# Optimization experiments

Measured on AMD Instinct MI355X. Metric: run time of the kernel, lower is better.

## Reference

```python
import jax, jax.numpy as jnp
import numpy as np

NUM_TIMESTEPS = 32
TOPK = 8


def setup_inputs() -> dict:
    key = jax.random.key(0)
    k = jax.random.split(key, 6)
    B, N, T, C = 16, 512, 32, 128
    r, d = C // 4, C // 2
    x_wav = jax.random.normal(k[0], (B, N, T, C), dtype=jnp.float32)
    # 1x1 Conv2d over channel dim == linear: weight [out_c, in_c]
    Ws = jax.random.normal(k[1], (r, C), dtype=jnp.float32) * 0.05   # W_shared, no bias
    Wphi = jax.random.normal(k[2], (C, r), dtype=jnp.float32) * 0.05
    b_phi = jnp.zeros((C,), dtype=jnp.float32)
    Wmu = jax.random.normal(k[3], (1, r), dtype=jnp.float32) * 0.05
    b_mu = jnp.zeros((1,), dtype=jnp.float32)
    WQ = jax.random.normal(k[4], (d, C), dtype=jnp.float32) * 0.05
    WK = jax.random.normal(k[5], (d, C), dtype=jnp.float32) * 0.05
    return {"x_wav": x_wav, "Ws": Ws, "Wphi": Wphi, "b_phi": b_phi,
            "Wmu": Wmu, "b_mu": b_mu, "WQ": WQ, "WK": WK}


def _row_topk(A, k):
    # keep the k largest entries per row (ties resolved by threshold;
    # with continuous sigmoid scores this matches torch's scatter mask)
    kth = jax.lax.top_k(A, k)[0][..., -1:]
    return A * (A >= kth).astype(A.dtype)


def reference(x_wav, Ws, Wphi, b_phi, Wmu, b_mu, WQ, WK):
    B, N, T, C = x_wav.shape
    T_delta = min(NUM_TIMESTEPS, T)
    X_w = x_wav[:, :, T - T_delta:, :]                       # [B,N,Td,C]
    # channel attention gate from time-averaged features
    avg = jnp.mean(X_w, axis=2, keepdims=True)               # [B,N,1,C]
    z_ca = jax.nn.relu(jnp.einsum('bntc,rc->bntr', avg, Ws))
    w = jax.nn.sigmoid(jnp.einsum('bntr,cr->bntc', z_ca, Wphi) + b_phi)  # [B,N,1,C]
    X_hat = X_w * w                                          # [B,N,Td,C]
    # temporal attention pooling
    z_ta = jax.nn.relu(jnp.einsum('bntc,rc->bntr', X_hat, Ws))
    logits = (jnp.einsum('bntr,or->bnto', z_ta, Wmu) + b_mu)[..., 0]     # [B,N,Td]
    alpha = jax.nn.softmax(logits, axis=2)
    X_c = jnp.einsum('bnt,bntc->bnc', alpha, X_hat)          # [B,N,C]
    # directed QK attention
    Q = jnp.einsum('bnc,dc->bnd', X_c, WQ)
    K = jnp.einsum('bnc,dc->bnd', X_c, WK)
    scale = jnp.sqrt(jnp.asarray(Q.shape[-1], dtype=X_c.dtype))
    E_f = jnp.einsum('bnd,bmd->bnm', Q, K) / scale
    E_b = jnp.einsum('bnd,bmd->bnm', K, Q) / scale
    S_f = _row_topk(jax.nn.sigmoid(E_f), TOPK)
    S_b = _row_topk(jax.nn.sigmoid(E_b), TOPK)
    return S_f, S_b
```

## Files before the change

### kernel.cpp

```cpp
#include <hip/hip_runtime.h>
#include <math.h>

#define BB 16
#define NN 512
#define TT 32
#define CC 128
#define RR 32
#define DD 64

__device__ __forceinline__ float dot_np16(const float* __restrict__ a,
                                          const float* __restrict__ b, int n) {
    float lane[16];
#pragma unroll
    for (int l = 0; l < 16; ++l) lane[l] = 0.0f;
    for (int i = 0; i < n; i += 16) {
#pragma unroll
        for (int l = 0; l < 16; ++l)
            lane[l] = __fmaf_rn(a[i + l], b[i + l], lane[l]);
    }
    float m[8], p[4];
#pragma unroll
    for (int i = 0; i < 8; ++i) m[i] = __fadd_rn(lane[i], lane[i + 8]);
#pragma unroll
    for (int i = 0; i < 4; ++i) p[i] = __fadd_rn(m[i], m[i + 4]);
    float q0 = __fadd_rn(p[0], p[2]);
    float q1 = __fadd_rn(p[1], p[3]);
    return __fadd_rn(q0, q1);
}

__device__ __forceinline__ float reduce_np16(const float (&lane)[16]) {
    float m[8], p[4];
#pragma unroll
    for (int i = 0; i < 8; ++i) m[i] = __fadd_rn(lane[i], lane[i + 8]);
#pragma unroll
    for (int i = 0; i < 4; ++i) p[i] = __fadd_rn(m[i], m[i + 4]);
    float q0 = __fadd_rn(p[0], p[2]);
    float q1 = __fadd_rn(p[1], p[3]);
    return __fadd_rn(q0, q1);
}

#define XS2 132

__global__ __launch_bounds__(256) void k1(const float* __restrict__ x,
        const float* __restrict__ Ws, const float* __restrict__ Wphi,
        const float* __restrict__ b_phi, const float* __restrict__ Wmu,
        const float* __restrict__ b_mu, const float* __restrict__ WQ,
        const float* __restrict__ WK,
        float* __restrict__ gQ, float* __restrict__ gK)
{
    __shared__ float Xs[TT * XS2];
    __shared__ float Wss[RR * XS2];
    __shared__ float zta[TT * 33];
    __shared__ float xc[CC];
    __shared__ float wsh[CC];
    __shared__ float zca[RR];
    __shared__ float lg[TT];
    __shared__ float alpha[TT];

    const int tid = threadIdx.x;
    const int bn = blockIdx.x;
    const float* xb = x + (long long)bn * (TT * CC);

#pragma unroll
    for (int k = 0; k < 4; ++k) {
        int idx = tid + (k << 8);
        int t  = idx >> 5;
        int c4 = (idx & 31) << 2;
        *(float4*)&Xs[t * XS2 + c4]  = ((const float4*)xb)[idx];
        *(float4*)&Wss[t * XS2 + c4] = ((const float4*)Ws)[idx];
    }
    __syncthreads();

    if (tid < CC) {
        float r[8];
#pragma unroll
        for (int j = 0; j < 8; ++j) r[j] = Xs[j * XS2 + tid];
#pragma unroll
        for (int i = 8; i < 32; i += 8)
#pragma unroll
            for (int j = 0; j < 8; ++j) r[j] = __fadd_rn(r[j], Xs[(i + j) * XS2 + tid]);
        float s = __fadd_rn(__fadd_rn(__fadd_rn(r[0], r[1]), __fadd_rn(r[2], r[3])),
                            __fadd_rn(__fadd_rn(r[4], r[5]), __fadd_rn(r[6], r[7])));
        xc[tid] = s / 32.0f;
    }
    __syncthreads();

    if (tid < RR) {
        const float* wr = &Wss[tid * XS2];
        float lane[16];
#pragma unroll
        for (int l = 0; l < 16; ++l) lane[l] = 0.0f;
#pragma unroll
        for (int c = 0; c < CC; c += 4) {
            float4 av = *(const float4*)&xc[c];
            float4 wv = *(const float4*)&wr[c];
            lane[(c & 15) + 0] = __fmaf_rn(av.x, wv.x, lane[(c & 15) + 0]);
            lane[(c & 15) + 1] = __fmaf_rn(av.y, wv.y, lane[(c & 15) + 1]);
            lane[(c & 15) + 2] = __fmaf_rn(av.z, wv.z, lane[(c & 15) + 2]);
            lane[(c & 15) + 3] = __fmaf_rn(av.w, wv.w, lane[(c & 15) + 3]);
        }
        zca[tid] = fmaxf(reduce_np16(lane), 0.0f);
    }
    __syncthreads();

    if (tid < CC) {
        float t = __fadd_rn(dot_np16(zca, Wphi + tid * RR, RR), b_phi[tid]);
        wsh[tid] = 1.0f / (1.0f + expf(-t));
    }
    __syncthreads();

#pragma unroll
    for (int k = 0; k < 16; ++k) {
        int i = tid + (k << 8);
        int t = i >> 7, c = i & 127;
        Xs[t * XS2 + c] = __fmul_rn(Xs[t * XS2 + c], wsh[c]);
    }
    __syncthreads();

    {
        const int t = tid & 31, q = tid >> 5;
        const float* xr = &Xs[t * XS2];
        float lane[4][16];
#pragma unroll
        for (int j = 0; j < 4; ++j)
#pragma unroll
            for (int l = 0; l < 16; ++l) lane[j][l] = 0.0f;
#pragma unroll
        for (int c = 0; c < CC; c += 4) {
            float4 xv = *(const float4*)&xr[c];
#pragma unroll
            for (int j = 0; j < 4; ++j) {
                float4 wv = *(const float4*)&Wss[(q + 8 * j) * XS2 + c];
                lane[j][(c & 15) + 0] = __fmaf_rn(xv.x, wv.x, lane[j][(c & 15) + 0]);
                lane[j][(c & 15) + 1] = __fmaf_rn(xv.y, wv.y, lane[j][(c & 15) + 1]);
                lane[j][(c & 15) + 2] = __fmaf_rn(xv.z, wv.z, lane[j][(c & 15) + 2]);
                lane[j][(c & 15) + 3] = __fmaf_rn(xv.w, wv.w, lane[j][(c & 15) + 3]);
            }
        }
#pragma unroll
        for (int j = 0; j < 4; ++j)
            zta[t * 33 + q + 8 * j] = fmaxf(reduce_np16(lane[j]), 0.0f);
    }
    __syncthreads();

    if (tid < TT) lg[tid] = __fadd_rn(dot_np16(&zta[tid * 33], Wmu, RR), b_mu[0]);
    __syncthreads();

    if (tid == 0) {
        float m = lg[0];
        for (int t = 1; t < TT; ++t) m = fmaxf(m, lg[t]);
        float e[TT];
        for (int t = 0; t < TT; ++t) e[t] = expf(__fsub_rn(lg[t], m));
        float r[8];
#pragma unroll
        for (int j = 0; j < 8; ++j) r[j] = e[j];
#pragma unroll
        for (int i = 8; i < 32; i += 8)
#pragma unroll
            for (int j = 0; j < 8; ++j) r[j] = __fadd_rn(r[j], e[i + j]);
        float s = __fadd_rn(__fadd_rn(__fadd_rn(r[0], r[1]), __fadd_rn(r[2], r[3])),
                            __fadd_rn(__fadd_rn(r[4], r[5]), __fadd_rn(r[6], r[7])));
        for (int t = 0; t < TT; ++t) alpha[t] = e[t] / s;
    }
    __syncthreads();

    if (tid < CC) {
        float s = 0.0f;
        for (int t = 0; t < TT; ++t)
            s = __fmaf_rn(alpha[t], Xs[t * XS2 + tid], s);
        xc[tid] = s;
    }
    __syncthreads();

    if (tid < 128) {
        int isK = tid >> 6, d = tid & 63;
        const float* Wr = (isK ? WK : WQ) + d * CC;
        float s = dot_np16(xc, Wr, CC);
        if (isK) gK[bn * DD + d] = s;
        else     gQ[bn * DD + d] = s;
    }
}

__device__ __forceinline__ void cxf(float& a, float& b) {
    float mx = fmaxf(a, b), mn = fminf(a, b);
    a = mx; b = mn;
}

#define KS 68

__global__ __launch_bounds__(256) void k2f(const float* __restrict__ gQ,
                                           const float* __restrict__ gK,
                                           float* __restrict__ out)
{
    __shared__ float Qs[16][64];
    __shared__ float Kch[64 * KS];

    const int tid = threadIdx.x;
    const int gid = blockIdx.x;
    const int dir = gid & 1;
    const int b   = (gid >> 1) & 15;
    const int grp = gid >> 5;
    const int row_base = grp << 4;

    const float* Qrow = dir ? gK : gQ;
    const float* Mat  = dir ? gQ : gK;
    float* outp = out + (long long)dir * BB * NN * NN;

    {
        int row = tid >> 4, c4 = (tid & 15) << 2;
        *(float4*)&Qs[row][c4] =
            ((const float4*)Qrow)[(long long)(b * NN + row_base + row) * 16 + (tid & 15)];
    }

    const int l = tid & 63, w = tid >> 6, wrow = w << 2;
    float A[4][8];

#pragma unroll
    for (int j = 0; j < 8; ++j) {
        __syncthreads();
#pragma unroll
        for (int k = 0; k < 4; ++k) {
            int idx = tid + (k << 8);
            int row = idx >> 4, c4 = (idx & 15) << 2;
            *(float4*)&Kch[row * KS + c4] =
                ((const float4*)Mat)[(long long)(b * NN + (j << 6) + row) * 16 + (idx & 15)];
        }
        __syncthreads();
#pragma unroll
        for (int r = 0; r < 4; ++r) {
            const float* qa = Qs[wrow + r];
            const float* kb = &Kch[l * KS];
            float lane[16];
#pragma unroll
            for (int ll = 0; ll < 16; ++ll) lane[ll] = 0.0f;
#pragma unroll
            for (int c = 0; c < DD; c += 4) {
                float4 qv = *(const float4*)&qa[c];
                float4 kv = *(const float4*)&kb[c];
                lane[(c & 15) + 0] = __fmaf_rn(qv.x, kv.x, lane[(c & 15) + 0]);
                lane[(c & 15) + 1] = __fmaf_rn(qv.y, kv.y, lane[(c & 15) + 1]);
                lane[(c & 15) + 2] = __fmaf_rn(qv.z, kv.z, lane[(c & 15) + 2]);
                lane[(c & 15) + 3] = __fmaf_rn(qv.w, kv.w, lane[(c & 15) + 3]);
            }
            float e = reduce_np16(lane);
            e = e / 8.0f;
            A[r][j] = 1.0f / (1.0f + expf(-e));
        }
    }

    const long long obase = (long long)(b * NN + row_base + wrow) * NN;

#pragma unroll
    for (int r = 0; r < 4; ++r) {
        float L[8];
#pragma unroll
        for (int j = 0; j < 8; ++j) L[j] = A[r][j];

        cxf(L[0],L[1]); cxf(L[2],L[3]); cxf(L[4],L[5]); cxf(L[6],L[7]);
        cxf(L[0],L[2]); cxf(L[1],L[3]); cxf(L[4],L[6]); cxf(L[5],L[7]);
        cxf(L[1],L[2]); cxf(L[5],L[6]);
        cxf(L[0],L[4]); cxf(L[1],L[5]); cxf(L[2],L[6]); cxf(L[3],L[7]);
        cxf(L[2],L[4]); cxf(L[3],L[5]);
        cxf(L[1],L[2]); cxf(L[3],L[4]); cxf(L[5],L[6]);

#pragma unroll
        for (int mask = 1; mask < 64; mask <<= 1) {
            float Pr[8], M[8];
#pragma unroll
            for (int j = 0; j < 8; ++j) Pr[j] = __shfl_xor(L[j], mask, 64);
#pragma unroll
            for (int j = 0; j < 8; ++j) M[j] = fmaxf(L[j], Pr[7 - j]);
            cxf(M[0],M[4]); cxf(M[1],M[5]); cxf(M[2],M[6]); cxf(M[3],M[7]);
            cxf(M[0],M[2]); cxf(M[1],M[3]); cxf(M[4],M[6]); cxf(M[5],M[7]);
            cxf(M[0],M[1]); cxf(M[2],M[3]); cxf(M[4],M[5]); cxf(M[6],M[7]);
#pragma unroll
            for (int j = 0; j < 8; ++j) L[j] = M[j];
        }
        const float kth = L[7];

        float* orow = outp + obase + (long long)r * NN;
#pragma unroll
        for (int j = 0; j < 8; ++j)
            orow[(j << 6) + l] = (A[r][j] >= kth) ? A[r][j] : 0.0f;
    }
}

extern "C" void kernel_launch(void* const* d_in, const int* in_sizes, int n_in,
                              void* d_out, int out_size, void* d_ws, size_t ws_size,
                              hipStream_t stream) {
    const float* x     = (const float*)d_in[0];
    const float* Ws    = (const float*)d_in[1];
    const float* Wphi  = (const float*)d_in[2];
    const float* b_phi = (const float*)d_in[3];
    const float* Wmu   = (const float*)d_in[4];
    const float* b_mu  = (const float*)d_in[5];
    const float* WQ    = (const float*)d_in[6];
    const float* WK    = (const float*)d_in[7];
    float* out = (float*)d_out;

    float* gQ = (float*)d_ws;
    float* gK = gQ + (long long)BB * NN * DD;

    hipLaunchKernelGGL(k1, dim3(8192), dim3(256), 0, stream,
                       x, Ws, Wphi, b_phi, Wmu, b_mu, WQ, WK, gQ, gK);
    hipLaunchKernelGGL(k2f, dim3(1024), dim3(256), 0, stream, gQ, gK, out);
}
```

Measured before the change: 196.2 us.

## Double k1 block size, split channel reduction, read Ws directly from global

Kernel k1 now runs 512 threads per block. The temporal-attention projection is split so that two half-waves each cover one half of the channel lanes, and the halves are combined with a cross-lane shuffle while keeping the same pairwise summation order. The shared-memory copy of Ws is removed; both Ws projections read the weights from global memory, where they are wave-uniform and cache-resident. The goal is lower shared-memory use, fewer registers per thread and more parallelism. The cost is extra global/L1 traffic and the risk that the unseen parts of the kernel assume 256 threads.

```diff
diff --git a/kernel.cpp b/kernel.cpp
--- a/kernel.cpp
+++ b/kernel.cpp
@@ -41,7 +41,7 @@
 
 #define XS2 132
 
-__global__ __launch_bounds__(256) void k1(const float* __restrict__ x,
+__global__ __launch_bounds__(512) void k1(const float* __restrict__ x,
         const float* __restrict__ Ws, const float* __restrict__ Wphi,
         const float* __restrict__ b_phi, const float* __restrict__ Wmu,
         const float* __restrict__ b_mu, const float* __restrict__ WQ,
@@ -49,7 +49,6 @@
         float* __restrict__ gQ, float* __restrict__ gK)
 {
     __shared__ float Xs[TT * XS2];
-    __shared__ float Wss[RR * XS2];
     __shared__ float zta[TT * 33];
     __shared__ float xc[CC];
     __shared__ float wsh[CC];
@@ -62,12 +61,11 @@
     const float* xb = x + (long long)bn * (TT * CC);
 
 #pragma unroll
-    for (int k = 0; k < 4; ++k) {
-        int idx = tid + (k << 8);
+    for (int k = 0; k < 2; ++k) {
+        int idx = tid + (k << 9);
         int t  = idx >> 5;
         int c4 = (idx & 31) << 2;
-        *(float4*)&Xs[t * XS2 + c4]  = ((const float4*)xb)[idx];
-        *(float4*)&Wss[t * XS2 + c4] = ((const float4*)Ws)[idx];
+        *(float4*)&Xs[t * XS2 + c4] = ((const float4*)xb)[idx];
     }
     __syncthreads();
 
@@ -86,7 +84,7 @@
     __syncthreads();
 
     if (tid < RR) {
-        const float* wr = &Wss[tid * XS2];
+        const float* wr = Ws + tid * CC;
         float lane[16];
 #pragma unroll
         for (int l = 0; l < 16; ++l) lane[l] = 0.0f;
@@ -110,36 +108,58 @@
     __syncthreads();
 
 #pragma unroll
-    for (int k = 0; k < 16; ++k) {
-        int i = tid + (k << 8);
+    for (int k = 0; k < 8; ++k) {
+        int i = tid + (k << 9);
         int t = i >> 7, c = i & 127;
         Xs[t * XS2 + c] = __fmul_rn(Xs[t * XS2 + c], wsh[c]);
     }
     __syncthreads();
 
     {
-        const int t = tid & 31, q = tid >> 5;
-        const float* xr = &Xs[t * XS2];
-        float lane[4][16];
+        const int t = tid & 31;
+        const int s = (tid >> 5) & 1;
+        const int wvid = tid >> 6;
+        const float* xr = &Xs[t * XS2 + 8 * s];
+        float acc[4][8];
 #pragma unroll
         for (int j = 0; j < 4; ++j)
 #pragma unroll
-            for (int l = 0; l < 16; ++l) lane[j][l] = 0.0f;
-#pragma unroll
-        for (int c = 0; c < CC; c += 4) {
-            float4 xv = *(const float4*)&xr[c];
+            for (int u = 0; u < 8; ++u) acc[j][u] = 0.0f;
+
+        for (int c = 0; c < CC; c += 16) {
+            float4 xv0 = *(const float4*)&xr[c];
+            float4 xv1 = *(const float4*)&xr[c + 4];
 #pragma unroll
             for (int j = 0; j < 4; ++j) {
-                float4 wv = *(const float4*)&Wss[(q + 8 * j) * XS2 + c];
-                lane[j][(c & 15) + 0] = __fmaf_rn(xv.x, wv.x, lane[j][(c & 15) + 0]);
-                lane[j][(c & 15) + 1] = __fmaf_rn(xv.y, wv.y, lane[j][(c & 15) + 1]);
-                lane[j][(c & 15) + 2] = __fmaf_rn(xv.z, wv.z, lane[j][(c & 15) + 2]);
-                lane[j][(c & 15) + 3] = __fmaf_rn(xv.w, wv.w, lane[j][(c & 15) + 3]);
+                const float* wp = Ws + (wvid + 8 * j) * CC + 8 * s + c;
+                float4 wv0 = *(const float4*)&wp[0];
+                float4 wv1 = *(const float4*)&wp[4];
+                acc[j][0] = __fmaf_rn(xv0.x, wv0.x, acc[j][0]);
+                acc[j][1] = __fmaf_rn(xv0.y, wv0.y, acc[j][1]);
+                acc[j][2] = __fmaf_rn(xv0.z, wv0.z, acc[j][2]);
+                acc[j][3] = __fmaf_rn(xv0.w, wv0.w, acc[j][3]);
+                acc[j][4] = __fmaf_rn(xv1.x, wv1.x, acc[j][4]);
+                acc[j][5] = __fmaf_rn(xv1.y, wv1.y, acc[j][5]);
+                acc[j][6] = __fmaf_rn(xv1.z, wv1.z, acc[j][6]);
+                acc[j][7] = __fmaf_rn(xv1.w, wv1.w, acc[j][7]);
             }
         }
 #pragma unroll
-        for (int j = 0; j < 4; ++j)
-            zta[t * 33 + q + 8 * j] = fmaxf(reduce_np16(lane[j]), 0.0f);
+        for (int j = 0; j < 4; ++j) {
+            float oth[8];
+#pragma unroll
+            for (int u = 0; u < 8; ++u) oth[u] = __shfl_xor(acc[j][u], 32, 64);
+            if (s == 0) {
+                float m[8], p[4];
+#pragma unroll
+                for (int u = 0; u < 8; ++u) m[u] = __fadd_rn(acc[j][u], oth[u]);
+#pragma unroll
+                for (int u = 0; u < 4; ++u) p[u] = __fadd_rn(m[u], m[u + 4]);
+                float q0 = __fadd_rn(p[0], p[2]);
+                float q1 = __fadd_rn(p[1], p[3]);
+                zta[t * 33 + wvid + 8 * j] = fmaxf(__fadd_rn(q0, q1), 0.0f);
+            }
+        }
     }
     __syncthreads();
 
@@ -301,7 +321,7 @@
     float* gQ = (float*)d_ws;
     float* gK = gQ + (long long)BB * NN * DD;
 
-    hipLaunchKernelGGL(k1, dim3(8192), dim3(256), 0, stream,
+    hipLaunchKernelGGL(k1, dim3(8192), dim3(512), 0, stream,
                        x, Ws, Wphi, b_phi, Wmu, b_mu, WQ, WK, gQ, gK);
     hipLaunchKernelGGL(k2f, dim3(1024), dim3(256), 0, stream, gQ, gK, out);
 }
```

New measurement: 504.9 us. 157% more time.
